# Optimization experiments

Measured on AMD Instinct MI355X. Metric: run time of the kernel, lower is better.

Reference implementation:

```python
import jax, jax.numpy as jnp
import numpy as np

TEMPERATURE = 0.5
EPS = 1e-12  # torch F.normalize eps


def setup_inputs() -> dict:
    key = jax.random.key(0)
    k1, k2 = jax.random.split(key)
    z_i = jax.random.normal(k1, (32, 128, 128), dtype=jnp.float32)
    z_j = jax.random.normal(k2, (32, 128, 128), dtype=jnp.float32)
    return {"z_i": z_i, "z_j": z_j}


def _l2_normalize(x):
    # matches torch F.normalize(dim=1): x / max(||x||, eps)
    n = jnp.sqrt(jnp.sum(x * x, axis=1, keepdims=True))
    return x / jnp.maximum(n, EPS)


def _off_diagonal(a):
    # rows of a with the diagonal removed, row-major order -> [n, n-1]
    n = a.shape[0]
    return a.reshape(-1)[:-1].reshape(n - 1, n + 1)[:, 1:].reshape(n, n - 1)


def reference(z_i, z_j):
    B, S, D = z_i.shape
    N = B * S
    zi = _l2_normalize(z_i.reshape(N, D))
    zj = _l2_normalize(z_j.reshape(N, D))
    r = jnp.concatenate([zi, zj], axis=0)              # [2N, D]
    sim = r @ r.T                                      # [2N, 2N]
    # positives: off-diagonals at +/-N (unaffected by the diag -inf fill)
    pos = jnp.concatenate([jnp.diagonal(sim, N), jnp.diagonal(sim, -N)])  # [2N]
    # negatives: all non-diagonal entries, row-major (== torch boolean-mask view)
    neg = _off_diagonal(sim)                           # [2N, 2N-1]
    logits = jnp.concatenate([pos[:, None], neg], axis=1) / TEMPERATURE  # [2N, 2N]
    # labels are all 0 -> CE(sum) / 2N == mean of -log_softmax[:, 0]
    loss = -jax.nn.log_softmax(logits, axis=1)[:, 0]
    return jnp.sum(loss) / (2 * N)
```

## Files before the change

### kernel.cpp

```cpp
#include <hip/hip_runtime.h>
#include <hip/hip_bf16.h>
#include <math.h>

#define NPAIR 4096
#define D 128
#define TWO_N 8192
#define NSLAB 32
#define ALPHA 1.6986436f

typedef float f32x4 __attribute__((ext_vector_type(4)));
typedef int i32x8 __attribute__((ext_vector_type(8)));

__device__ __forceinline__ void async_ld16(void* lds, const void* g) {
    __builtin_amdgcn_global_load_lds(
        (__attribute__((address_space(1))) const unsigned int*)g,
        (__attribute__((address_space(3))) unsigned int*)lds, 16, 0, 0);
}

__device__ __forceinline__ i32x8 mk8(uint4 lo, uint4 hi) {
    return (i32x8){(int)lo.x, (int)lo.y, (int)lo.z, (int)lo.w,
                   (int)hi.x, (int)hi.y, (int)hi.z, (int)hi.w};
}

__global__ __launch_bounds__(256) void norm_kernel(const float* __restrict__ zi,
                                                   const float* __restrict__ zj,
                                                   unsigned char* __restrict__ Rb,
                                                   float* __restrict__ pos,
                                                   float* __restrict__ out) {
    if (blockIdx.x == 0 && threadIdx.x == 0) out[0] = 0.f;
    int k = blockIdx.x * 8 + (threadIdx.x >> 5);
    int t = threadIdx.x & 31;
    const float4 a = *(const float4*)(zi + k * D + 4 * t);
    const float4 b = *(const float4*)(zj + k * D + 4 * t);
    float si = a.x * a.x + a.y * a.y + a.z * a.z + a.w * a.w;
    float sj = b.x * b.x + b.y * b.y + b.z * b.z + b.w * b.w;
    float dt = a.x * b.x + a.y * b.y + a.z * b.z + a.w * b.w;
    #pragma unroll
    for (int m = 1; m < 32; m <<= 1) {
        si += __shfl_xor(si, m, 32);
        sj += __shfl_xor(sj, m, 32);
        dt += __shfl_xor(dt, m, 32);
    }
    float ii = 1.0f / fmaxf(sqrtf(si), 1e-12f);
    float ij = 1.0f / fmaxf(sqrtf(sj), 1e-12f);
    if (t == 0) pos[k] = dt * ii * ij;
    ii *= ALPHA; ij *= ALPHA;
    int r0 = __builtin_amdgcn_cvt_pk_fp8_f32(a.x * ii, a.y * ii, 0, false);
    r0 = __builtin_amdgcn_cvt_pk_fp8_f32(a.z * ii, a.w * ii, r0, true);
    *(unsigned int*)(Rb + (size_t)k * 128 + 4 * t) = (unsigned int)r0;
    int r1 = __builtin_amdgcn_cvt_pk_fp8_f32(b.x * ij, b.y * ij, 0, false);
    r1 = __builtin_amdgcn_cvt_pk_fp8_f32(b.z * ij, b.w * ij, r1, true);
    *(unsigned int*)(Rb + (size_t)(k + NPAIR) * 128 + 4 * t) = (unsigned int)r1;
}

__global__ __launch_bounds__(256, 4) void simexp_kernel(const unsigned char* __restrict__ Rb,
                                                        float* __restrict__ rspart) {
    __shared__ uint4 Bs[4][3][128];
    const int bi = blockIdx.x >> 3;
    const int jc = blockIdx.x & 7;
    const int tid = threadIdx.x;
    const int wave = tid >> 6, lane = tid & 63;
    const int rp = lane & 15, q = lane >> 4;

    i32x8 afr[4];
    {
        const unsigned char* Ab = Rb + (size_t)(bi * 64 + rp) * 128 + q * 32;
        #pragma unroll
        for (int rt = 0; rt < 4; ++rt) {
            uint4 h0 = *(const uint4*)(Ab + rt * 16 * 128);
            uint4 h1 = *(const uint4*)(Ab + rt * 16 * 128 + 16);
            afr[rt] = mk8(h0, h1);
        }
    }

    const unsigned char* gslab = Rb + (size_t)(jc * 1024 + wave * 16) * 128;
    char* lpanel = (char*)&Bs[wave][0][0];
    const int laneoff = (lane >> 3) * 128 + (((lane & 7) ^ ((lane >> 3) & 7)) << 4);

    float rs[16];
    #pragma unroll
    for (int i = 0; i < 16; ++i) rs[i] = 0.f;

    #pragma unroll
    for (int j = 0; j < 2; ++j)
        #pragma unroll
        for (int d = 0; d < 2; ++d)
            async_ld16(lpanel + j * 2048 + d * 1024,
                       gslab + j * 8192 + d * 1024 + laneoff);

    const int diagbase = bi * 64 - jc * 1024;
    const int slot0 = rp * 8;
    const int sw = rp & 7;

    f32x4 z0 = {0.f, 0.f, 0.f, 0.f};

    #pragma unroll
    for (int jt = 0; jt < 16; ++jt) {
        if (jt < 14) __builtin_amdgcn_s_waitcnt(0x0F72);
        else         __builtin_amdgcn_s_waitcnt(0x0F70);

        const int cur = jt % 3;
        const uint4* P = &Bs[wave][cur][0];
        uint4 u0 = P[slot0 + ((q * 2 + 0) ^ sw)];
        uint4 u1 = P[slot0 + ((q * 2 + 1) ^ sw)];
        i32x8 bfr = mk8(u0, u1);

        if (jt < 14) {
            const int nb = (jt + 2) % 3;
            #pragma unroll
            for (int d = 0; d < 2; ++d)
                async_ld16(lpanel + nb * 2048 + d * 1024,
                           gslab + (jt + 2) * 8192 + d * 1024 + laneoff);
        }

        f32x4 acc[4];
        __builtin_amdgcn_s_setprio(1);
        #pragma unroll
        for (int rt = 0; rt < 4; ++rt)
            acc[rt] = __builtin_amdgcn_mfma_scale_f32_16x16x128_f8f6f4(
                afr[rt], bfr, z0,
                0, 0,
                0, 0x7F7F7F7F,
                0, 0x7F7F7F7F);
        __builtin_amdgcn_s_setprio(0);

        if (jt * 64 == diagbase) {
            #pragma unroll
            for (int rt = 0; rt < 4; ++rt)
                #pragma unroll
                for (int r = 0; r < 4; ++r) {
                    int ro = rt * 16 + q * 4 + r;
                    int co = wave * 16 + rp;
                    float e = __builtin_amdgcn_exp2f(acc[rt][r]);
                    rs[rt * 4 + r] += (ro == co) ? 0.f : e;
                }
        } else {
            #pragma unroll
            for (int rt = 0; rt < 4; ++rt)
                #pragma unroll
                for (int r = 0; r < 4; ++r)
                    rs[rt * 4 + r] += __builtin_amdgcn_exp2f(acc[rt][r]);
        }
    }

    #pragma unroll
    for (int i = 0; i < 16; ++i) {
        float v = rs[i];
        v += __shfl_xor(v, 1, 64);
        v += __shfl_xor(v, 2, 64);
        v += __shfl_xor(v, 4, 64);
        v += __shfl_xor(v, 8, 64);
        rs[i] = v;
    }
    if (rp == 0) {
        const int slab = jc * 4 + wave;
        const int rowb = bi * 64 + q * 4;
        #pragma unroll
        for (int rt = 0; rt < 4; ++rt)
            #pragma unroll
            for (int r = 0; r < 4; ++r)
                rspart[(size_t)(rowb + rt * 16 + r) * NSLAB + slab] = rs[rt * 4 + r];
    }
}

__global__ __launch_bounds__(128) void finalize_kernel(const float* __restrict__ rspart,
                                                       const float* __restrict__ pos,
                                                       float* __restrict__ out) {
    __shared__ float red[2];
    int tid = threadIdx.x;
    int k = blockIdx.x * 128 + tid;
    const f32x4* v = (const f32x4*)(rspart + (size_t)k * NSLAB);
    f32x4 s = v[0];
    #pragma unroll
    for (int p = 1; p < 8; ++p) s += v[p];
    float rsum = s.x + s.y + s.z + s.w;
    float ps = pos[k & (NPAIR - 1)];
    float p2 = ps + ps;
    float local = logf(rsum + __expf(p2)) - p2;
    #pragma unroll
    for (int m = 1; m < 64; m <<= 1) local += __shfl_xor(local, m, 64);
    if ((tid & 63) == 0) red[tid >> 6] = local;
    __syncthreads();
    if (tid == 0) atomicAdd(out, (red[0] + red[1]) * (1.0f / (float)TWO_N));
}

extern "C" void kernel_launch(void* const* d_in, const int* in_sizes, int n_in,
                              void* d_out, int out_size, void* d_ws, size_t ws_size,
                              hipStream_t stream) {
    const float* zi = (const float*)d_in[0];
    const float* zj = (const float*)d_in[1];
    char* ws = (char*)d_ws;
    unsigned char* Rb = (unsigned char*)ws;
    float* rspart = (float*)(ws + 1 * 1024 * 1024);
    float* pos = (float*)(ws + 2 * 1024 * 1024);

    norm_kernel<<<NPAIR / 8, 256, 0, stream>>>(zi, zj, Rb, pos, (float*)d_out);
    simexp_kernel<<<128 * 8, 256, 0, stream>>>(Rb, rspart);
    finalize_kernel<<<64, 128, 0, stream>>>(rspart, pos, (float*)d_out);
}
```

Baseline: 78.30 us.

## Fuse finalize reduction into sim kernel via last-blocks atomic counter

Removes the separate finalize kernel launch. Each sim block increments a global counter after writing its partial row sums. The last 64 blocks to arrive spin until every block is done, then each reduces one slice of rows and atomically adds its slice to the output. The change also drops the s_setprio hints and the shared zero accumulator in the MFMA loop. This saves a launch and its gap but adds a spin-wait, which depends on all blocks being co-resident or finishing without deadlock.

```diff
diff --git a/kernel.cpp b/kernel.cpp
--- a/kernel.cpp
+++ b/kernel.cpp
@@ -6,6 +6,8 @@
 #define D 128
 #define TWO_N 8192
 #define NSLAB 32
+#define NBLK 1024
+#define NFIN 64
 #define ALPHA 1.6986436f
 
 typedef float f32x4 __attribute__((ext_vector_type(4)));
@@ -26,8 +28,9 @@
                                                    const float* __restrict__ zj,
                                                    unsigned char* __restrict__ Rb,
                                                    float* __restrict__ pos,
+                                                   int* __restrict__ cnt,
                                                    float* __restrict__ out) {
-    if (blockIdx.x == 0 && threadIdx.x == 0) out[0] = 0.f;
+    if (blockIdx.x == 0 && threadIdx.x == 0) { out[0] = 0.f; *cnt = 0; }
     int k = blockIdx.x * 8 + (threadIdx.x >> 5);
     int t = threadIdx.x & 31;
     const float4 a = *(const float4*)(zi + k * D + 4 * t);
@@ -53,9 +56,14 @@
     *(unsigned int*)(Rb + (size_t)(k + NPAIR) * 128 + 4 * t) = (unsigned int)r1;
 }
 
-__global__ __launch_bounds__(256, 4) void simexp_kernel(const unsigned char* __restrict__ Rb,
-                                                        float* __restrict__ rspart) {
+__global__ __launch_bounds__(256, 4) void simfin_kernel(const unsigned char* __restrict__ Rb,
+                                                        float* __restrict__ rspart,
+                                                        const float* __restrict__ pos,
+                                                        int* __restrict__ cnt,
+                                                        float* __restrict__ out) {
     __shared__ uint4 Bs[4][3][128];
+    __shared__ float red[4];
+    __shared__ int sOld;
     const int bi = blockIdx.x >> 3;
     const int jc = blockIdx.x & 7;
     const int tid = threadIdx.x;
@@ -92,8 +100,6 @@
     const int slot0 = rp * 8;
     const int sw = rp & 7;
 
-    f32x4 z0 = {0.f, 0.f, 0.f, 0.f};
-
     #pragma unroll
     for (int jt = 0; jt < 16; ++jt) {
         if (jt < 14) __builtin_amdgcn_s_waitcnt(0x0F72);
@@ -113,16 +119,14 @@
                            gslab + (jt + 2) * 8192 + d * 1024 + laneoff);
         }
 
-        f32x4 acc[4];
-        __builtin_amdgcn_s_setprio(1);
+        f32x4 acc[4] = {};
         #pragma unroll
         for (int rt = 0; rt < 4; ++rt)
             acc[rt] = __builtin_amdgcn_mfma_scale_f32_16x16x128_f8f6f4(
-                afr[rt], bfr, z0,
+                afr[rt], bfr, acc[rt],
                 0, 0,
                 0, 0x7F7F7F7F,
                 0, 0x7F7F7F7F);
-        __builtin_amdgcn_s_setprio(0);
 
         if (jt * 64 == diagbase) {
             #pragma unroll
@@ -161,27 +165,38 @@
             for (int r = 0; r < 4; ++r)
                 rspart[(size_t)(rowb + rt * 16 + r) * NSLAB + slab] = rs[rt * 4 + r];
     }
-}
-
-__global__ __launch_bounds__(128) void finalize_kernel(const float* __restrict__ rspart,
-                                                       const float* __restrict__ pos,
-                                                       float* __restrict__ out) {
-    __shared__ float red[2];
-    int tid = threadIdx.x;
-    int k = blockIdx.x * 128 + tid;
-    const f32x4* v = (const f32x4*)(rspart + (size_t)k * NSLAB);
-    f32x4 s = v[0];
-    #pragma unroll
-    for (int p = 1; p < 8; ++p) s += v[p];
-    float rsum = s.x + s.y + s.z + s.w;
-    float ps = pos[k & (NPAIR - 1)];
-    float p2 = ps + ps;
-    float local = logf(rsum + __expf(p2)) - p2;
+
+    __threadfence();
+    if (tid == 0) sOld = atomicAdd(cnt, 1);
+    __syncthreads();
+    const int old = sOld;
+    if (old < NBLK - NFIN) return;
+    const int slice = old - (NBLK - NFIN);
+    if (tid == 0) {
+        while (__hip_atomic_load(cnt, __ATOMIC_ACQUIRE, __HIP_MEMORY_SCOPE_AGENT) < NBLK)
+            __builtin_amdgcn_s_sleep(2);
+    }
+    __syncthreads();
+    __threadfence();
+
+    float local = 0.f;
+    if (tid < 128) {
+        const int k = slice * 128 + tid;
+        const f32x4* v = (const f32x4*)(rspart + (size_t)k * NSLAB);
+        f32x4 s4 = v[0];
+        #pragma unroll
+        for (int p = 1; p < 8; ++p) s4 += v[p];
+        float rsum = s4.x + s4.y + s4.z + s4.w;
+        float ps = pos[k & (NPAIR - 1)];
+        float p2 = ps + ps;
+        local = logf(rsum + __expf(p2)) - p2;
+    }
     #pragma unroll
     for (int m = 1; m < 64; m <<= 1) local += __shfl_xor(local, m, 64);
     if ((tid & 63) == 0) red[tid >> 6] = local;
     __syncthreads();
-    if (tid == 0) atomicAdd(out, (red[0] + red[1]) * (1.0f / (float)TWO_N));
+    if (tid == 0)
+        atomicAdd(out, (red[0] + red[1] + red[2] + red[3]) * (1.0f / (float)TWO_N));
 }
 
 extern "C" void kernel_launch(void* const* d_in, const int* in_sizes, int n_in,
@@ -193,8 +208,8 @@
     unsigned char* Rb = (unsigned char*)ws;
     float* rspart = (float*)(ws + 1 * 1024 * 1024);
     float* pos = (float*)(ws + 2 * 1024 * 1024);
-
-    norm_kernel<<<NPAIR / 8, 256, 0, stream>>>(zi, zj, Rb, pos, (float*)d_out);
-    simexp_kernel<<<128 * 8, 256, 0, stream>>>(Rb, rspart);
-    finalize_kernel<<<64, 128, 0, stream>>>(rspart, pos, (float*)d_out);
-}
+    int* cnt = (int*)(ws + 2 * 1024 * 1024 + 16 * 1024);
+
+    norm_kernel<<<NPAIR / 8, 256, 0, stream>>>(zi, zj, Rb, pos, cnt, (float*)d_out);
+    simfin_kernel<<<NBLK, 256, 0, stream>>>(Rb, rspart, pos, cnt, (float*)d_out);
+}
```

Measured after the change: 205.1 us. +161.9%, slower.
